# Kernel tuning notes

Hardware: AMD Instinct MI355X
Metric: run time of the kernel (lower is better)

Reference implementation:

```python
import jax, jax.numpy as jnp
import numpy as np

N = 512

def setup_inputs() -> dict:
    key = jax.random.key(0)
    ks = jax.random.split(key, 7)
    def rn(k, shape, fan_in):
        # kaiming-ish scale so activations stay sane
        return jax.random.normal(k, shape, dtype=jnp.float32) / np.sqrt(max(fan_in, 1))
    return {
        "x": jax.random.normal(ks[0], (N,), dtype=jnp.float32),
        "W1": rn(ks[1], (2, 1024), 2),
        "b1": rn(ks[2], (1024,), 1024),
        "W2": rn(ks[3], (1024, 128), 1024),
        "b2": rn(ks[4], (128,), 128),
        "W3": rn(ks[5], (128, 1), 128),
        "b3": rn(ks[6], (1,), 1),
    }


def reference(x, W1, b1, W2, b2, W3, b3):
    n = x.shape[0]
    # all (t_i, t_j) pairs: [N, N, 2]
    pairs = jnp.stack(
        [jnp.broadcast_to(x[:, None], (n, n)),
         jnp.broadcast_to(x[None, :], (n, n))], axis=-1)
    # batched 3-layer MLP over all pairs
    h = jax.nn.relu(jnp.einsum("ijc,ch->ijh", pairs, W1) + b1)   # [N,N,1024]
    h = jax.nn.relu(jnp.einsum("ijh,hk->ijk", h, W2) + b2)       # [N,N,128]
    out = (jnp.einsum("ijk,ko->ijo", h, W3) + b3)[..., 0]        # [N,N]
    # original fills only j >= i (diagonal overwritten from eye); lower stays 0
    K = jnp.triu(out)
    return K.T @ K
```

## Files before the change

### kernel.cpp

```cpp
#include <hip/hip_runtime.h>
#include <hip/hip_fp16.h>

typedef _Float16 f16;
typedef _Float16 f16x8 __attribute__((ext_vector_type(8)));
typedef float f32x4 __attribute__((ext_vector_type(4)));

__device__ __forceinline__ f16x8 relu8(f16x8 a) {
#if __has_builtin(__builtin_elementwise_max)
  return __builtin_elementwise_max(a, (f16x8)(f16)0);
#else
  f16x8 r;
#pragma unroll
  for (int i = 0; i < 8; i++) r[i] = a[i] > (f16)0 ? a[i] : (f16)0;
  return r;
#endif
}

__device__ __forceinline__ f16x8 bcast8(f16 s) {
  return (f16x8){s, s, s, s, s, s, s, s};
}

__global__ __launch_bounds__(512, 2) void k_fused(
    const float* __restrict__ x, const float* __restrict__ W1,
    const float* __restrict__ b1, const float* __restrict__ b2,
    const float* __restrict__ W3, const float* __restrict__ b3,
    const float* __restrict__ W2,
    float* __restrict__ Kp0, float* __restrict__ Kp1) {
  __shared__ f16 w2f[65536];
  __shared__ f16 w1af[1024], b1f[1024], w1bf[1024];
  __shared__ f16 hat[8192];
  __shared__ f16 xs[512];

  const int tid = threadIdx.x;
  const int lane = tid & 63, wv = tid >> 6;
  const int cL = lane & 15, q = lane >> 4;

  if (tid < 128) {
    const int c8 = tid << 3;
    const float4 a0 = *(const float4*)(W1 + c8);
    const float4 a1 = *(const float4*)(W1 + c8 + 4);
    const float4 g0 = *(const float4*)(b1 + c8);
    const float4 g1 = *(const float4*)(b1 + c8 + 4);
    f16x8 oa, og;
    oa[0] = (f16)a0.x; oa[1] = (f16)a0.y; oa[2] = (f16)a0.z; oa[3] = (f16)a0.w;
    oa[4] = (f16)a1.x; oa[5] = (f16)a1.y; oa[6] = (f16)a1.z; oa[7] = (f16)a1.w;
    og[0] = (f16)g0.x; og[1] = (f16)g0.y; og[2] = (f16)g0.z; og[3] = (f16)g0.w;
    og[4] = (f16)g1.x; og[5] = (f16)g1.y; og[6] = (f16)g1.z; og[7] = (f16)g1.w;
    *(f16x8*)(&w1af[c8]) = oa;
    *(f16x8*)(&b1f[c8]) = og;
  } else if (tid < 256) {
    const int c8 = (tid - 128) << 3;
    const float4 a0 = *(const float4*)(W1 + 1024 + c8);
    const float4 a1 = *(const float4*)(W1 + 1024 + c8 + 4);
    f16x8 ob;
    ob[0] = (f16)a0.x; ob[1] = (f16)a0.y; ob[2] = (f16)a0.z; ob[3] = (f16)a0.w;
    ob[4] = (f16)a1.x; ob[5] = (f16)a1.y; ob[6] = (f16)a1.z; ob[7] = (f16)a1.w;
    *(f16x8*)(&w1bf[c8]) = ob;
  } else if (tid < 320) {
    const int c8 = (tid - 256) << 3;
    const float4 x0 = *(const float4*)(x + c8);
    const float4 x1 = *(const float4*)(x + c8 + 4);
    f16x8 ox;
    ox[0] = (f16)x0.x; ox[1] = (f16)x0.y; ox[2] = (f16)x0.z; ox[3] = (f16)x0.w;
    ox[4] = (f16)x1.x; ox[5] = (f16)x1.y; ox[6] = (f16)x1.z; ox[7] = (f16)x1.w;
    *(f16x8*)(&xs[c8]) = ox;
  }

  int cur_nh = -1;

  for (int t = (int)blockIdx.x; t < 320; t += 256) {
    int nh, jt, s;
    if (t < 64 || t >= 256) {
      const int b = (t < 64) ? t : (t - 256);
      nh = b & 1;
      const int jd = b >> 1;
      const int jt1 = jd >> 4, l = jd & 15;
      if (t < 64) { jt = jt1;            s = jt * 16 + l; }
      else        { jt = (jt1 + 2) & 3;  s = jt * 16 + (15 - l); }
    } else {
      const int f = t - 64;
      nh = f & 1;
      const int jf = f >> 1;
      if (jf < 16)      { jt = 1; s = jf; }
      else if (jf < 48) { jt = 2; s = jf - 16; }
      else              { jt = 3; s = jf - 48; }
    }
    const int i0 = s << 3, j0 = jt << 7;
    float* __restrict__ Kp = nh ? Kp1 : Kp0;

    __syncthreads();
    if (nh != cur_nh) {
      #pragma unroll
      for (int p = 0; p < 16; p++) {
        const int sl = p * 512 + tid;
        const int frag = sl >> 6, l = sl & 63;
        const int cgL = frag >> 5, kb2 = frag & 31;
        const int q2 = l >> 4, cL2 = l & 15;
        const int n = nh * 64 + cgL * 16 + cL2;
        const float* src = W2 + (kb2 * 32 + q2 * 8) * 128 + n;
        f16x8 o;
        #pragma unroll
        for (int e = 0; e < 8; e++) o[e] = (f16)src[e * 128];
        *(f16x8*)(&w2f[frag * 512 + l * 8]) = o;
      }
      cur_nh = nh;
    }
    {
      const int il_s = tid >> 6, kb = (tid & 63) << 4;
      const f16x8 xv = bcast8(xs[i0 + il_s]);
      const f16x8 wa0 = *(const f16x8*)(&w1af[kb]);
      const f16x8 wa1 = *(const f16x8*)(&w1af[kb + 8]);
      const f16x8 bb0 = *(const f16x8*)(&b1f[kb]);
      const f16x8 bb1 = *(const f16x8*)(&b1f[kb + 8]);
      *(f16x8*)(&hat[il_s * 1024 + kb])     = xv * wa0 + bb0;
      *(f16x8*)(&hat[il_s * 1024 + kb + 8]) = xv * wa1 + bb1;
    }
    __syncthreads();

    const int i = i0 + wv;
    const int dij = i - j0;
    const int rgmin = (dij > 0) ? (dij >> 4) : 0;

    f16 xjs[8];
    #pragma unroll
    for (int rg = 0; rg < 8; rg++) xjs[rg] = xs[j0 + rg * 16 + cL];

    f32x4 acc[8][4];
    #pragma unroll
    for (int rg = 0; rg < 8; rg++)
      #pragma unroll
      for (int cg = 0; cg < 4; cg++) acc[rg][cg] = (f32x4){0.f, 0.f, 0.f, 0.f};

    const f16* hrow  = hat + wv * 1024 + q * 8;
    const f16* wrow  = w1bf + q * 8;
    const f16* bbase = w2f + lane * 8;

    for (int kk = 0; kk < 32; ++kk) {
      const f16x8 hv = *(const f16x8*)(hrow + kk * 32);
      const f16x8 wb = *(const f16x8*)(wrow + kk * 32);
      f16x8 bf[4];
      #pragma unroll
      for (int cg = 0; cg < 4; cg++)
        bf[cg] = *(const f16x8*)(bbase + (cg * 32 + kk) * 512);
      #pragma unroll
      for (int rg = 0; rg < 8; rg++) {
        if (rg >= rgmin) {
          const f16x8 af = relu8(bcast8(xjs[rg]) * wb + hv);
          #pragma unroll
          for (int cg = 0; cg < 4; cg++)
            acc[rg][cg] = __builtin_amdgcn_mfma_f32_16x16x32_f16(af, bf[cg], acc[rg][cg], 0, 0, 0);
        }
      }
    }

    float b2v[4], w3v[4];
    #pragma unroll
    for (int cg = 0; cg < 4; cg++) {
      b2v[cg] = b2[nh * 64 + cg * 16 + cL];
      w3v[cg] = W3[nh * 64 + cg * 16 + cL];
    }
    const float badd = (nh == 0) ? b3[0] : 0.f;
    #pragma unroll
    for (int rg = 0; rg < 8; rg++) {
      if (rg >= rgmin) {
        #pragma unroll
        for (int r = 0; r < 4; r++) {
          float ssum = 0.f;
          #pragma unroll
          for (int cg = 0; cg < 4; cg++)
            ssum = fmaf(fmaxf(acc[rg][cg][r] + b2v[cg], 0.f), w3v[cg], ssum);
          ssum += __shfl_xor(ssum, 1, 64);
          ssum += __shfl_xor(ssum, 2, 64);
          ssum += __shfl_xor(ssum, 4, 64);
          ssum += __shfl_xor(ssum, 8, 64);
          if (cL == 0) {
            const int j = j0 + rg * 16 + q * 4 + r;
            if (j >= i) Kp[i * 512 + j] = ssum + badd;
          }
        }
      }
    }
  }
}

__global__ __launch_bounds__(256) void k_atta2(const float* __restrict__ K0,
                                               const float* __restrict__ K1,
                                               float* __restrict__ C) {
  __shared__ __align__(16) float sp[2][32 * 36];
  __shared__ __align__(16) float sq[2][32 * 36];

  int a = 0, rem = (int)blockIdx.x;
  #pragma unroll
  for (int aa = 0; aa < 16; aa++) {
    const int c = 16 - aa;
    if (rem < c) { a = aa; break; }
    rem -= c;
  }
  const int b = a + rem;
  const int pb = a * 32, qb = b * 32;
  const int nchunk = a + 1;

  const int tid = threadIdx.x;
  const int ii = tid >> 3, p4 = (tid & 7) << 2;
  const int tx = tid & 15, ty = tid >> 4;

  float4 x0, x1, y0, y1;
  {
    const int gp = ii * 512 + pb + p4, gq = ii * 512 + qb + p4;
    x0 = *(const float4*)(K0 + gp);
    x1 = *(const float4*)(K1 + gp);
    y0 = *(const float4*)(K0 + gq);
    y1 = *(const float4*)(K1 + gq);
  }

  float c00 = 0.f, c01 = 0.f, c10 = 0.f, c11 = 0.f;

  for (int ic = 0; ic < nchunk; ic++) {
    float* __restrict__ spb = sp[ic & 1];
    float* __restrict__ sqb = sq[ic & 1];
    const int r = ic * 32 + ii;
    float4 vp, vq;
    vp.x = (r <= pb + p4 + 0) ? x0.x + x1.x : 0.f;
    vp.y = (r <= pb + p4 + 1) ? x0.y + x1.y : 0.f;
    vp.z = (r <= pb + p4 + 2) ? x0.z + x1.z : 0.f;
    vp.w = (r <= pb + p4 + 3) ? x0.w + x1.w : 0.f;
    vq.x = (r <= qb + p4 + 0) ? y0.x + y1.x : 0.f;
    vq.y = (r <= qb + p4 + 1) ? y0.y + y1.y : 0.f;
    vq.z = (r <= qb + p4 + 2) ? y0.z + y1.z : 0.f;
    vq.w = (r <= qb + p4 + 3) ? y0.w + y1.w : 0.f;
    *(float4*)&spb[ii * 36 + p4] = vp;
    *(float4*)&sqb[ii * 36 + p4] = vq;
    __syncthreads();

    if (ic + 1 < nchunk) {
      const int r2 = (ic + 1) * 32 + ii;
      const int gp = r2 * 512 + pb + p4, gq = r2 * 512 + qb + p4;
      x0 = *(const float4*)(K0 + gp);
      x1 = *(const float4*)(K1 + gp);
      y0 = *(const float4*)(K0 + gq);
      y1 = *(const float4*)(K1 + gq);
    }

    #pragma unroll 8
    for (int k = 0; k < 32; k++) {
      const float2 av = *(const float2*)&spb[k * 36 + ty * 2];
      const float2 bv = *(const float2*)&sqb[k * 36 + tx * 2];
      c00 = fmaf(av.x, bv.x, c00); c01 = fmaf(av.x, bv.y, c01);
      c10 = fmaf(av.y, bv.x, c10); c11 = fmaf(av.y, bv.y, c11);
    }
  }

  const int p0 = pb + ty * 2, q0 = qb + tx * 2;
  *(float2*)&C[p0 * 512 + q0]       = make_float2(c00, c01);
  *(float2*)&C[(p0 + 1) * 512 + q0] = make_float2(c10, c11);
  if (pb != qb) {
    *(float2*)&C[q0 * 512 + p0]       = make_float2(c00, c10);
    *(float2*)&C[(q0 + 1) * 512 + p0] = make_float2(c01, c11);
  }
}

extern "C" void kernel_launch(void* const* d_in, const int* in_sizes, int n_in,
                              void* d_out, int out_size, void* d_ws, size_t ws_size,
                              hipStream_t stream) {
  const float* x  = (const float*)d_in[0];
  const float* W1 = (const float*)d_in[1];
  const float* b1 = (const float*)d_in[2];
  const float* W2 = (const float*)d_in[3];
  const float* b2 = (const float*)d_in[4];
  const float* W3 = (const float*)d_in[5];
  const float* b3 = (const float*)d_in[6];
  float* out = (float*)d_out;
  char* ws = (char*)d_ws;

  float* Kp0 = (float*)ws;
  float* Kp1 = (float*)(ws + (1 << 20));

  k_fused<<<256, 512, 0, stream>>>(x, W1, b1, b2, W3, b3, W2, Kp0, Kp1);
  k_atta2<<<136, 256, 0, stream>>>(Kp0, Kp1, out);
}
```

Before: 119.2 us.

## Split MLP tile into two half passes with double-buffered LDS loads and MFMA priority

The 8x4 MFMA accumulator tile per wave is split into two sequential passes of 4x4, which halves accumulator register pressure and skips whole passes below the diagonal. Each pass software-pipelines its LDS loads (h, W1b, W2 fragments) one k-step ahead and raises wave priority around the MFMA groups. The cost is that W2 and h fragments are reloaded from LDS once per half, and the extra template specialisation adds code size.

Result: no change. 121.1 us (+1.6%).

```diff
diff --git a/kernel.cpp b/kernel.cpp
--- a/kernel.cpp
+++ b/kernel.cpp
@@ -2,6 +2,7 @@
 #include <hip/hip_fp16.h>
 
 typedef _Float16 f16;
+typedef _Float16 f16x4 __attribute__((ext_vector_type(4)));
 typedef _Float16 f16x8 __attribute__((ext_vector_type(8)));
 typedef float f32x4 __attribute__((ext_vector_type(4)));
 
@@ -18,6 +19,48 @@
 
 __device__ __forceinline__ f16x8 bcast8(f16 s) {
   return (f16x8){s, s, s, s, s, s, s, s};
+}
+
+struct Acc16 { f32x4 a[16]; };
+
+template <bool GUARD>
+__device__ __forceinline__ Acc16 mlp_pass(
+    const f16* __restrict__ hrow, const f16* __restrict__ wrow,
+    const f16* __restrict__ bbase, const f16x4 xj, const int rgeff) {
+  Acc16 A;
+#pragma unroll
+  for (int t = 0; t < 16; t++) A.a[t] = (f32x4){0.f, 0.f, 0.f, 0.f};
+
+  f16x8 hvb[2], wbb[2], bfb[2][4];
+  hvb[0] = *(const f16x8*)(hrow);
+  wbb[0] = *(const f16x8*)(wrow);
+#pragma unroll
+  for (int cg = 0; cg < 4; cg++)
+    bfb[0][cg] = *(const f16x8*)(bbase + (cg * 32) * 512);
+
+#pragma unroll 2
+  for (int kk = 0; kk < 32; ++kk) {
+    const int cur = kk & 1, nxt = cur ^ 1;
+    const int kn = (kk < 31) ? (kk + 1) : 31;
+    hvb[nxt] = *(const f16x8*)(hrow + kn * 32);
+    wbb[nxt] = *(const f16x8*)(wrow + kn * 32);
+#pragma unroll
+    for (int cg = 0; cg < 4; cg++)
+      bfb[nxt][cg] = *(const f16x8*)(bbase + (cg * 32 + kn) * 512);
+#pragma unroll
+    for (int rg = 0; rg < 4; rg++) {
+      if (!GUARD || rg >= rgeff) {
+        const f16x8 af = relu8(bcast8(xj[rg]) * wbb[cur] + hvb[cur]);
+        __builtin_amdgcn_s_setprio(1);
+#pragma unroll
+        for (int cg = 0; cg < 4; cg++)
+          A.a[rg * 4 + cg] = __builtin_amdgcn_mfma_f32_16x16x32_f16(
+              af, bfb[cur][cg], A.a[rg * 4 + cg], 0, 0, 0);
+        __builtin_amdgcn_s_setprio(0);
+      }
+    }
+  }
+  return A;
 }
 
 __global__ __launch_bounds__(512, 2) void k_fused(
@@ -121,37 +164,9 @@
     const int dij = i - j0;
     const int rgmin = (dij > 0) ? (dij >> 4) : 0;
 
-    f16 xjs[8];
-    #pragma unroll
-    for (int rg = 0; rg < 8; rg++) xjs[rg] = xs[j0 + rg * 16 + cL];
-
-    f32x4 acc[8][4];
-    #pragma unroll
-    for (int rg = 0; rg < 8; rg++)
-      #pragma unroll
-      for (int cg = 0; cg < 4; cg++) acc[rg][cg] = (f32x4){0.f, 0.f, 0.f, 0.f};
-
     const f16* hrow  = hat + wv * 1024 + q * 8;
     const f16* wrow  = w1bf + q * 8;
     const f16* bbase = w2f + lane * 8;
-
-    for (int kk = 0; kk < 32; ++kk) {
-      const f16x8 hv = *(const f16x8*)(hrow + kk * 32);
-      const f16x8 wb = *(const f16x8*)(wrow + kk * 32);
-      f16x8 bf[4];
-      #pragma unroll
-      for (int cg = 0; cg < 4; cg++)
-        bf[cg] = *(const f16x8*)(bbase + (cg * 32 + kk) * 512);
-      #pragma unroll
-      for (int rg = 0; rg < 8; rg++) {
-        if (rg >= rgmin) {
-          const f16x8 af = relu8(bcast8(xjs[rg]) * wb + hv);
-          #pragma unroll
-          for (int cg = 0; cg < 4; cg++)
-            acc[rg][cg] = __builtin_amdgcn_mfma_f32_16x16x32_f16(af, bf[cg], acc[rg][cg], 0, 0, 0);
-        }
-      }
-    }
 
     float b2v[4], w3v[4];
     #pragma unroll
@@ -160,22 +175,36 @@
       w3v[cg] = W3[nh * 64 + cg * 16 + cL];
     }
     const float badd = (nh == 0) ? b3[0] : 0.f;
-    #pragma unroll
-    for (int rg = 0; rg < 8; rg++) {
-      if (rg >= rgmin) {
-        #pragma unroll
-        for (int r = 0; r < 4; r++) {
-          float ssum = 0.f;
+
+    for (int half = 0; half < 2; ++half) {
+      const int rb = half << 2;
+      if (rgmin >= rb + 4) continue;
+
+      f16x4 xj;
+      #pragma unroll
+      for (int rg = 0; rg < 4; rg++) xj[rg] = xs[j0 + (rb + rg) * 16 + cL];
+
+      Acc16 A = (rgmin <= rb)
+                    ? mlp_pass<false>(hrow, wrow, bbase, xj, 0)
+                    : mlp_pass<true>(hrow, wrow, bbase, xj, rgmin - rb);
+
+      #pragma unroll
+      for (int rg = 0; rg < 4; rg++) {
+        if (rb + rg >= rgmin) {
           #pragma unroll
-          for (int cg = 0; cg < 4; cg++)
-            ssum = fmaf(fmaxf(acc[rg][cg][r] + b2v[cg], 0.f), w3v[cg], ssum);
-          ssum += __shfl_xor(ssum, 1, 64);
-          ssum += __shfl_xor(ssum, 2, 64);
-          ssum += __shfl_xor(ssum, 4, 64);
-          ssum += __shfl_xor(ssum, 8, 64);
-          if (cL == 0) {
-            const int j = j0 + rg * 16 + q * 4 + r;
-            if (j >= i) Kp[i * 512 + j] = ssum + badd;
+          for (int r = 0; r < 4; r++) {
+            float ssum = 0.f;
+            #pragma unroll
+            for (int cg = 0; cg < 4; cg++)
+              ssum = fmaf(fmaxf(A.a[rg * 4 + cg][r] + b2v[cg], 0.f), w3v[cg], ssum);
+            ssum += __shfl_xor(ssum, 1, 64);
+            ssum += __shfl_xor(ssum, 2, 64);
+            ssum += __shfl_xor(ssum, 4, 64);
+            ssum += __shfl_xor(ssum, 8, 64);
+            if (cL == 0) {
+              const int j = j0 + (rb + rg) * 16 + q * 4 + r;
+              if (j >= i) Kp[i * 512 + j] = ssum + badd;
+            }
           }
         }
       }
```

## Split N-columns of fused MLP across two waves per row with LDS reduction

Applied to the files above, without the earlier changes.

Doubles the block size to 1024 threads so each row i is handled by two waves, each computing half of the 64 output columns (2 MFMA column groups instead of 4). Partial layer-3 dot products are written to shared memory (reusing the hat buffer) and summed by one wave before the store. This halves accumulator registers per wave and doubles wave-level parallelism to hide MFMA and LDS latency. The cost is an extra barrier and an LDS reduction per tile, and the relu'd A fragment is now recomputed by both waves.

Measured after the change: 134.4 us. 1.13x slower.

```diff
diff --git a/kernel.cpp b/kernel.cpp
--- a/kernel.cpp
+++ b/kernel.cpp
@@ -20,7 +20,7 @@
   return (f16x8){s, s, s, s, s, s, s, s};
 }
 
-__global__ __launch_bounds__(512, 2) void k_fused(
+__global__ __launch_bounds__(1024, 4) void k_fused(
     const float* __restrict__ x, const float* __restrict__ W1,
     const float* __restrict__ b1, const float* __restrict__ b2,
     const float* __restrict__ W3, const float* __restrict__ b3,
@@ -32,7 +32,10 @@
   __shared__ f16 xs[512];
 
   const int tid = threadIdx.x;
-  const int lane = tid & 63, wv = tid >> 6;
+  const int lane = tid & 63;
+  const int wv16 = tid >> 6;
+  const int il = wv16 >> 1;
+  const int cgh = wv16 & 1;
   const int cL = lane & 15, q = lane >> 4;
 
   if (tid < 128) {
@@ -91,8 +94,8 @@
     __syncthreads();
     if (nh != cur_nh) {
       #pragma unroll
-      for (int p = 0; p < 16; p++) {
-        const int sl = p * 512 + tid;
+      for (int p = 0; p < 8; p++) {
+        const int sl = p * 1024 + tid;
         const int frag = sl >> 6, l = sl & 63;
         const int cgL = frag >> 5, kb2 = frag & 31;
         const int q2 = l >> 4, cL2 = l & 15;
@@ -106,18 +109,15 @@
       cur_nh = nh;
     }
     {
-      const int il_s = tid >> 6, kb = (tid & 63) << 4;
+      const int il_s = tid >> 7, kb = (tid & 127) << 3;
       const f16x8 xv = bcast8(xs[i0 + il_s]);
-      const f16x8 wa0 = *(const f16x8*)(&w1af[kb]);
-      const f16x8 wa1 = *(const f16x8*)(&w1af[kb + 8]);
-      const f16x8 bb0 = *(const f16x8*)(&b1f[kb]);
-      const f16x8 bb1 = *(const f16x8*)(&b1f[kb + 8]);
-      *(f16x8*)(&hat[il_s * 1024 + kb])     = xv * wa0 + bb0;
-      *(f16x8*)(&hat[il_s * 1024 + kb + 8]) = xv * wa1 + bb1;
-    }
-    __syncthreads();
-
-    const int i = i0 + wv;
+      const f16x8 wa = *(const f16x8*)(&w1af[kb]);
+      const f16x8 bb = *(const f16x8*)(&b1f[kb]);
+      *(f16x8*)(&hat[il_s * 1024 + kb]) = xv * wa + bb;
+    }
+    __syncthreads();
+
+    const int i = i0 + il;
     const int dij = i - j0;
     const int rgmin = (dij > 0) ? (dij >> 4) : 0;
 
@@ -125,59 +125,69 @@
     #pragma unroll
     for (int rg = 0; rg < 8; rg++) xjs[rg] = xs[j0 + rg * 16 + cL];
 
-    f32x4 acc[8][4];
-    #pragma unroll
-    for (int rg = 0; rg < 8; rg++)
-      #pragma unroll
-      for (int cg = 0; cg < 4; cg++) acc[rg][cg] = (f32x4){0.f, 0.f, 0.f, 0.f};
-
-    const f16* hrow  = hat + wv * 1024 + q * 8;
+    f32x4 acc[8][2];
+    #pragma unroll
+    for (int rg = 0; rg < 8; rg++) {
+      acc[rg][0] = (f32x4){0.f, 0.f, 0.f, 0.f};
+      acc[rg][1] = (f32x4){0.f, 0.f, 0.f, 0.f};
+    }
+
+    const f16* hrow  = hat + il * 1024 + q * 8;
     const f16* wrow  = w1bf + q * 8;
-    const f16* bbase = w2f + lane * 8;
+    const f16* bbase = w2f + cgh * 32768 + lane * 8;
 
     for (int kk = 0; kk < 32; ++kk) {
       const f16x8 hv = *(const f16x8*)(hrow + kk * 32);
       const f16x8 wb = *(const f16x8*)(wrow + kk * 32);
-      f16x8 bf[4];
-      #pragma unroll
-      for (int cg = 0; cg < 4; cg++)
-        bf[cg] = *(const f16x8*)(bbase + (cg * 32 + kk) * 512);
+      const f16x8 bf0 = *(const f16x8*)(bbase + kk * 512);
+      const f16x8 bf1 = *(const f16x8*)(bbase + 16384 + kk * 512);
       #pragma unroll
       for (int rg = 0; rg < 8; rg++) {
         if (rg >= rgmin) {
           const f16x8 af = relu8(bcast8(xjs[rg]) * wb + hv);
-          #pragma unroll
-          for (int cg = 0; cg < 4; cg++)
-            acc[rg][cg] = __builtin_amdgcn_mfma_f32_16x16x32_f16(af, bf[cg], acc[rg][cg], 0, 0, 0);
+          acc[rg][0] = __builtin_amdgcn_mfma_f32_16x16x32_f16(af, bf0, acc[rg][0], 0, 0, 0);
+          acc[rg][1] = __builtin_amdgcn_mfma_f32_16x16x32_f16(af, bf1, acc[rg][1], 0, 0, 0);
         }
       }
     }
 
-    float b2v[4], w3v[4];
-    #pragma unroll
-    for (int cg = 0; cg < 4; cg++) {
-      b2v[cg] = b2[nh * 64 + cg * 16 + cL];
-      w3v[cg] = W3[nh * 64 + cg * 16 + cL];
-    }
-    const float badd = (nh == 0) ? b3[0] : 0.f;
+    float b2v[2], w3v[2];
+    #pragma unroll
+    for (int c = 0; c < 2; c++) {
+      const int n = nh * 64 + (cgh * 2 + c) * 16 + cL;
+      b2v[c] = b2[n];
+      w3v[c] = W3[n];
+    }
+
+    __syncthreads();
+    float* part = (float*)hat;
+
     #pragma unroll
     for (int rg = 0; rg < 8; rg++) {
       if (rg >= rgmin) {
         #pragma unroll
         for (int r = 0; r < 4; r++) {
-          float ssum = 0.f;
-          #pragma unroll
-          for (int cg = 0; cg < 4; cg++)
-            ssum = fmaf(fmaxf(acc[rg][cg][r] + b2v[cg], 0.f), w3v[cg], ssum);
+          float ssum = fmaf(fmaxf(acc[rg][0][r] + b2v[0], 0.f), w3v[0],
+                       fmaxf(acc[rg][1][r] + b2v[1], 0.f) * w3v[1]);
           ssum += __shfl_xor(ssum, 1, 64);
           ssum += __shfl_xor(ssum, 2, 64);
           ssum += __shfl_xor(ssum, 4, 64);
           ssum += __shfl_xor(ssum, 8, 64);
-          if (cL == 0) {
-            const int j = j0 + rg * 16 + q * 4 + r;
-            if (j >= i) Kp[i * 512 + j] = ssum + badd;
-          }
+          if (cL == 0)
+            part[(cgh * 8 + il) * 128 + rg * 16 + q * 4 + r] = ssum;
         }
+      }
+    }
+    __syncthreads();
+
+    if (cgh == 0) {
+      const float badd = (nh == 0) ? b3[0] : 0.f;
+      #pragma unroll
+      for (int jj0 = 0; jj0 < 128; jj0 += 64) {
+        const int jj = jj0 + lane;
+        const int j = j0 + jj;
+        if (j >= i)
+          Kp[i * 512 + j] = part[il * 128 + jj] + part[(8 + il) * 128 + jj] + badd;
       }
     }
   }
@@ -275,6 +285,6 @@
   float* Kp0 = (float*)ws;
   float* Kp1 = (float*)(ws + (1 << 20));
 
-  k_fused<<<256, 512, 0, stream>>>(x, W1, b1, b2, W3, b3, W2, Kp0, Kp1);
+  k_fused<<<256, 1024, 0, stream>>>(x, W1, b1, b2, W3, b3, W2, Kp0, Kp1);
   k_atta2<<<136, 256, 0, stream>>>(Kp0, Kp1, out);
 }
```

## Replace per-pair MLP with piecewise-linear sweep over sorted x breakpoints

Applied to the files above, without the earlier changes.

For a fixed i, the first-layer activation of each hidden unit is piecewise linear in x_j and has a single ReLU breakpoint. The new code sorts x once in a prep kernel, then builds per-row event lists of hidden units bucketed by breakpoint. A sweep across the sorted x_j keeps running prefix sums A and B of the W2 columns, so the second layer costs O(1024·128) per row instead of one MFMA GEMM per pair. This removes the dense fp16 MFMA work and the two-half partial K buffers. In exchange it adds a bitonic sort, atomics-based bucketing, a serial sweep whose work differs between waves, scattered stores back to unsorted column positions, and fp32 accumulation order that differs from the reference.

New measurement: 295.3 us. 2.48x slower.

```diff
diff --git a/kernel.cpp b/kernel.cpp
--- a/kernel.cpp
+++ b/kernel.cpp
@@ -2,195 +2,251 @@
 #include <hip/hip_fp16.h>
 
 typedef _Float16 f16;
+typedef _Float16 f16x2 __attribute__((ext_vector_type(2)));
 typedef _Float16 f16x8 __attribute__((ext_vector_type(8)));
-typedef float f32x4 __attribute__((ext_vector_type(4)));
-
-__device__ __forceinline__ f16x8 relu8(f16x8 a) {
-#if __has_builtin(__builtin_elementwise_max)
-  return __builtin_elementwise_max(a, (f16x8)(f16)0);
-#else
-  f16x8 r;
-#pragma unroll
-  for (int i = 0; i < 8; i++) r[i] = a[i] > (f16)0 ? a[i] : (f16)0;
-  return r;
-#endif
+
+#define WS_XS 0
+#define WS_JO 2048
+#define WS_W2H 4096
+#define WS_K (1 << 19)
+
+__global__ __launch_bounds__(512) void k_prep(const float* __restrict__ x,
+                                              const float* __restrict__ W2,
+                                              char* __restrict__ ws) {
+  __shared__ float xv[512];
+  __shared__ int xj[512];
+  const int tid = threadIdx.x;
+  xv[tid] = x[tid];
+  xj[tid] = tid;
+  __syncthreads();
+  for (int k2 = 2; k2 <= 512; k2 <<= 1) {
+    for (int j2 = k2 >> 1; j2 >= 1; j2 >>= 1) {
+      const int partner = tid ^ j2;
+      if (partner > tid) {
+        const bool asc = ((tid & k2) == 0);
+        const float a = xv[tid], b = xv[partner];
+        const bool sw = asc ? (a > b) : (a < b);
+        if (sw) {
+          xv[tid] = b; xv[partner] = a;
+          const int ja = xj[tid]; xj[tid] = xj[partner]; xj[partner] = ja;
+        }
+      }
+      __syncthreads();
+    }
+  }
+  ((float*)(ws + WS_XS))[tid] = xv[tid];
+  ((int*)(ws + WS_JO))[tid] = xj[tid];
+
+  f16* __restrict__ w2h = (f16*)(ws + WS_W2H);
+  for (int base = tid * 8; base < 1024 * 128; base += 512 * 8) {
+    const float4 a = *(const float4*)(W2 + base);
+    const float4 b = *(const float4*)(W2 + base + 4);
+    f16x8 o;
+    o[0] = (f16)a.x; o[1] = (f16)a.y; o[2] = (f16)a.z; o[3] = (f16)a.w;
+    o[4] = (f16)b.x; o[5] = (f16)b.y; o[6] = (f16)b.z; o[7] = (f16)b.w;
+    *(f16x8*)(w2h + base) = o;
+  }
 }
 
-__device__ __forceinline__ f16x8 bcast8(f16 s) {
-  return (f16x8){s, s, s, s, s, s, s, s};
-}
-
-__global__ __launch_bounds__(512, 2) void k_fused(
+__global__ __launch_bounds__(256, 2) void k_sweep(
     const float* __restrict__ x, const float* __restrict__ W1,
     const float* __restrict__ b1, const float* __restrict__ b2,
     const float* __restrict__ W3, const float* __restrict__ b3,
-    const float* __restrict__ W2,
-    float* __restrict__ Kp0, float* __restrict__ Kp1) {
-  __shared__ f16 w2f[65536];
-  __shared__ f16 w1af[1024], b1f[1024], w1bf[1024];
-  __shared__ f16 hat[8192];
-  __shared__ f16 xs[512];
+    const char* __restrict__ ws, float* __restrict__ Kf) {
+  __shared__ float xsp[512];
+  __shared__ int jof[512];
+  __shared__ float evc[2048], evt[2048];
+  __shared__ unsigned short evk[2048];
+  __shared__ int startS[513];
+  __shared__ int histS[513];
+  __shared__ float chkA[4][128], chkB[4][128];
+  __shared__ float outls[512];
 
   const int tid = threadIdx.x;
   const int lane = tid & 63, wv = tid >> 6;
-  const int cL = lane & 15, q = lane >> 4;
-
-  if (tid < 128) {
-    const int c8 = tid << 3;
-    const float4 a0 = *(const float4*)(W1 + c8);
-    const float4 a1 = *(const float4*)(W1 + c8 + 4);
-    const float4 g0 = *(const float4*)(b1 + c8);
-    const float4 g1 = *(const float4*)(b1 + c8 + 4);
-    f16x8 oa, og;
-    oa[0] = (f16)a0.x; oa[1] = (f16)a0.y; oa[2] = (f16)a0.z; oa[3] = (f16)a0.w;
-    oa[4] = (f16)a1.x; oa[5] = (f16)a1.y; oa[6] = (f16)a1.z; oa[7] = (f16)a1.w;
-    og[0] = (f16)g0.x; og[1] = (f16)g0.y; og[2] = (f16)g0.z; og[3] = (f16)g0.w;
-    og[4] = (f16)g1.x; og[5] = (f16)g1.y; og[6] = (f16)g1.z; og[7] = (f16)g1.w;
-    *(f16x8*)(&w1af[c8]) = oa;
-    *(f16x8*)(&b1f[c8]) = og;
-  } else if (tid < 256) {
-    const int c8 = (tid - 128) << 3;
-    const float4 a0 = *(const float4*)(W1 + 1024 + c8);
-    const float4 a1 = *(const float4*)(W1 + 1024 + c8 + 4);
-    f16x8 ob;
-    ob[0] = (f16)a0.x; ob[1] = (f16)a0.y; ob[2] = (f16)a0.z; ob[3] = (f16)a0.w;
-    ob[4] = (f16)a1.x; ob[5] = (f16)a1.y; ob[6] = (f16)a1.z; ob[7] = (f16)a1.w;
-    *(f16x8*)(&w1bf[c8]) = ob;
-  } else if (tid < 320) {
-    const int c8 = (tid - 256) << 3;
-    const float4 x0 = *(const float4*)(x + c8);
-    const float4 x1 = *(const float4*)(x + c8 + 4);
-    f16x8 ox;
-    ox[0] = (f16)x0.x; ox[1] = (f16)x0.y; ox[2] = (f16)x0.z; ox[3] = (f16)x0.w;
-    ox[4] = (f16)x1.x; ox[5] = (f16)x1.y; ox[6] = (f16)x1.z; ox[7] = (f16)x1.w;
-    *(f16x8*)(&xs[c8]) = ox;
-  }
-
-  int cur_nh = -1;
-
-  for (int t = (int)blockIdx.x; t < 320; t += 256) {
-    int nh, jt, s;
-    if (t < 64 || t >= 256) {
-      const int b = (t < 64) ? t : (t - 256);
-      nh = b & 1;
-      const int jd = b >> 1;
-      const int jt1 = jd >> 4, l = jd & 15;
-      if (t < 64) { jt = jt1;            s = jt * 16 + l; }
-      else        { jt = (jt1 + 2) & 3;  s = jt * 16 + (15 - l); }
-    } else {
-      const int f = t - 64;
-      nh = f & 1;
-      const int jf = f >> 1;
-      if (jf < 16)      { jt = 1; s = jf; }
-      else if (jf < 48) { jt = 2; s = jf - 16; }
-      else              { jt = 3; s = jf - 48; }
-    }
-    const int i0 = s << 3, j0 = jt << 7;
-    float* __restrict__ Kp = nh ? Kp1 : Kp0;
-
-    __syncthreads();
-    if (nh != cur_nh) {
-      #pragma unroll
-      for (int p = 0; p < 16; p++) {
-        const int sl = p * 512 + tid;
-        const int frag = sl >> 6, l = sl & 63;
-        const int cgL = frag >> 5, kb2 = frag & 31;
-        const int q2 = l >> 4, cL2 = l & 15;
-        const int n = nh * 64 + cgL * 16 + cL2;
-        const float* src = W2 + (kb2 * 32 + q2 * 8) * 128 + n;
-        f16x8 o;
-        #pragma unroll
-        for (int e = 0; e < 8; e++) o[e] = (f16)src[e * 128];
-        *(f16x8*)(&w2f[frag * 512 + l * 8]) = o;
-      }
-      cur_nh = nh;
-    }
-    {
-      const int il_s = tid >> 6, kb = (tid & 63) << 4;
-      const f16x8 xv = bcast8(xs[i0 + il_s]);
-      const f16x8 wa0 = *(const f16x8*)(&w1af[kb]);
-      const f16x8 wa1 = *(const f16x8*)(&w1af[kb + 8]);
-      const f16x8 bb0 = *(const f16x8*)(&b1f[kb]);
-      const f16x8 bb1 = *(const f16x8*)(&b1f[kb + 8]);
-      *(f16x8*)(&hat[il_s * 1024 + kb])     = xv * wa0 + bb0;
-      *(f16x8*)(&hat[il_s * 1024 + kb + 8]) = xv * wa1 + bb1;
-    }
-    __syncthreads();
-
-    const int i = i0 + wv;
-    const int dij = i - j0;
-    const int rgmin = (dij > 0) ? (dij >> 4) : 0;
-
-    f16 xjs[8];
-    #pragma unroll
-    for (int rg = 0; rg < 8; rg++) xjs[rg] = xs[j0 + rg * 16 + cL];
-
-    f32x4 acc[8][4];
-    #pragma unroll
-    for (int rg = 0; rg < 8; rg++)
-      #pragma unroll
-      for (int cg = 0; cg < 4; cg++) acc[rg][cg] = (f32x4){0.f, 0.f, 0.f, 0.f};
-
-    const f16* hrow  = hat + wv * 1024 + q * 8;
-    const f16* wrow  = w1bf + q * 8;
-    const f16* bbase = w2f + lane * 8;
-
-    for (int kk = 0; kk < 32; ++kk) {
-      const f16x8 hv = *(const f16x8*)(hrow + kk * 32);
-      const f16x8 wb = *(const f16x8*)(wrow + kk * 32);
-      f16x8 bf[4];
-      #pragma unroll
-      for (int cg = 0; cg < 4; cg++)
-        bf[cg] = *(const f16x8*)(bbase + (cg * 32 + kk) * 512);
-      #pragma unroll
-      for (int rg = 0; rg < 8; rg++) {
-        if (rg >= rgmin) {
-          const f16x8 af = relu8(bcast8(xjs[rg]) * wb + hv);
-          #pragma unroll
-          for (int cg = 0; cg < 4; cg++)
-            acc[rg][cg] = __builtin_amdgcn_mfma_f32_16x16x32_f16(af, bf[cg], acc[rg][cg], 0, 0, 0);
+  const int i = (int)blockIdx.x;
+  const float xi = x[i];
+  const f16* __restrict__ w2h = (const f16*)(ws + WS_W2H);
+
+  {
+    const float* xsg = (const float*)(ws + WS_XS);
+    const int* jog = (const int*)(ws + WS_JO);
+    xsp[tid] = xsg[tid];       xsp[tid + 256] = xsg[tid + 256];
+    jof[tid] = jog[tid];       jof[tid + 256] = jog[tid + 256];
+    histS[tid] = 0;            histS[tid + 256] = 0;
+    if (tid == 0) histS[512] = 0;
+  }
+  __syncthreads();
+
+  float kc[4], kt[4];
+  int kpos[4];
+#pragma unroll
+  for (int r = 0; r < 4; r++) {
+    const int k = tid + 256 * r;
+    const float a = W1[k], c = W1[1024 + k], b = b1[k];
+    const float t = fmaf(a, xi, b);
+    kc[r] = c; kt[r] = t;
+    int pos = 0;
+    if (c != 0.f) {
+      const float bp = -t / c;
+#pragma unroll
+      for (int s = 256; s > 0; s >>= 1)
+        if (pos + s <= 512 && xsp[pos + s - 1] < bp) pos += s;
+    }
+    kpos[r] = pos;
+    if (c > 0.f) {
+      atomicAdd(&histS[pos], 1);
+    } else if (c < 0.f) {
+      atomicAdd(&histS[0], 1);
+      atomicAdd(&histS[pos], 1);
+    } else if (t > 0.f) {
+      atomicAdd(&histS[0], 1);
+    }
+  }
+  __syncthreads();
+
+  if (wv == 0) {
+    int hloc[8], s8 = 0;
+#pragma unroll
+    for (int u = 0; u < 8; u++) { hloc[u] = histS[lane * 8 + u]; s8 += hloc[u]; }
+    int incl = s8;
+#pragma unroll
+    for (int d = 1; d < 64; d <<= 1) {
+      const int o = __shfl_up(incl, d, 64);
+      if (lane >= d) incl += o;
+    }
+    int run = incl - s8;
+#pragma unroll
+    for (int u = 0; u < 8; u++) { startS[lane * 8 + u] = run; run += hloc[u]; }
+    if (lane == 63) startS[512] = incl;
+  }
+  __syncthreads();
+  histS[tid] = startS[tid];
+  histS[tid + 256] = startS[tid + 256];
+  if (tid == 0) histS[512] = startS[512];
+  __syncthreads();
+
+#pragma unroll
+  for (int r = 0; r < 4; r++) {
+    const int k = tid + 256 * r;
+    const float c = kc[r], t = kt[r];
+    if (c > 0.f) {
+      const int sl = atomicAdd(&histS[kpos[r]], 1);
+      evc[sl] = c; evt[sl] = t; evk[sl] = (unsigned short)k;
+    } else if (c < 0.f) {
+      int sl = atomicAdd(&histS[0], 1);
+      evc[sl] = c; evt[sl] = t; evk[sl] = (unsigned short)k;
+      sl = atomicAdd(&histS[kpos[r]], 1);
+      evc[sl] = -c; evt[sl] = -t; evk[sl] = (unsigned short)k;
+    } else if (t > 0.f) {
+      const int sl = atomicAdd(&histS[0], 1);
+      evc[sl] = 0.f; evt[sl] = t; evk[sl] = (unsigned short)k;
+    }
+  }
+  __syncthreads();
+
+  const int n0 = 2 * lane;
+  const float b2n0 = b2[n0], b2n1 = b2[n0 + 1];
+  const float w3n0 = W3[n0], w3n1 = W3[n0 + 1];
+
+  const int csBeg = startS[wv * 128];
+  const int csEnd = startS[(wv + 1) * 128];
+
+  {
+    float dA0 = 0.f, dB0 = 0.f, dA1 = 0.f, dB1 = 0.f;
+    for (int e = csBeg; e < csEnd; e += 8) {
+      float pc[8], pt[8], pw0[8], pw1[8];
+#pragma unroll
+      for (int u = 0; u < 8; u++) {
+        const int idx = min(e + u, 2047);
+        pc[u] = evc[idx]; pt[u] = evt[idx];
+        const int k = evk[idx] & 1023;
+        const f16x2 wp = *(const f16x2*)(w2h + k * 128 + n0);
+        pw0[u] = (float)wp[0]; pw1[u] = (float)wp[1];
+      }
+#pragma unroll
+      for (int u = 0; u < 8; u++) {
+        if (e + u < csEnd) {
+          dA0 = fmaf(pc[u], pw0[u], dA0); dB0 = fmaf(pt[u], pw0[u], dB0);
+          dA1 = fmaf(pc[u], pw1[u], dA1); dB1 = fmaf(pt[u], pw1[u], dB1);
         }
       }
     }
-
-    float b2v[4], w3v[4];
-    #pragma unroll
-    for (int cg = 0; cg < 4; cg++) {
-      b2v[cg] = b2[nh * 64 + cg * 16 + cL];
-      w3v[cg] = W3[nh * 64 + cg * 16 + cL];
-    }
-    const float badd = (nh == 0) ? b3[0] : 0.f;
-    #pragma unroll
-    for (int rg = 0; rg < 8; rg++) {
-      if (rg >= rgmin) {
-        #pragma unroll
-        for (int r = 0; r < 4; r++) {
-          float ssum = 0.f;
-          #pragma unroll
-          for (int cg = 0; cg < 4; cg++)
-            ssum = fmaf(fmaxf(acc[rg][cg][r] + b2v[cg], 0.f), w3v[cg], ssum);
-          ssum += __shfl_xor(ssum, 1, 64);
-          ssum += __shfl_xor(ssum, 2, 64);
-          ssum += __shfl_xor(ssum, 4, 64);
-          ssum += __shfl_xor(ssum, 8, 64);
-          if (cL == 0) {
-            const int j = j0 + rg * 16 + q * 4 + r;
-            if (j >= i) Kp[i * 512 + j] = ssum + badd;
+    chkA[wv][n0] = dA0; chkA[wv][n0 + 1] = dA1;
+    chkB[wv][n0] = dB0; chkB[wv][n0 + 1] = dB1;
+  }
+  __syncthreads();
+
+  float A0 = 0.f, B0 = 0.f, A1 = 0.f, B1 = 0.f;
+  for (int u = 0; u < wv; u++) {
+    A0 += chkA[u][n0]; A1 += chkA[u][n0 + 1];
+    B0 += chkB[u][n0]; B1 += chkB[u][n0 + 1];
+  }
+
+  {
+    int p = wv * 128;
+    const int p1 = p + 128;
+    int e = csBeg;
+    const int eEnd = csEnd;
+    int nextB = startS[p + 1];
+
+    auto EMIT = [&](int pp) {
+      const float xp = xsp[pp];
+      float v = fmaxf(fmaf(A0, xp, B0) + b2n0, 0.f) * w3n0 +
+                fmaxf(fmaf(A1, xp, B1) + b2n1, 0.f) * w3n1;
+#pragma unroll
+      for (int d = 1; d < 64; d <<= 1) v += __shfl_xor(v, d, 64);
+      if (lane == 0) outls[pp] = v;
+    };
+
+    while (p < p1) {
+      while (p < p1 && nextB <= e) {
+        EMIT(p); p++;
+        if (p < p1) nextB = startS[p + 1];
+      }
+      if (p >= p1) break;
+      float pc[8], pt[8], pw0[8], pw1[8];
+#pragma unroll
+      for (int u = 0; u < 8; u++) {
+        const int idx = min(e + u, 2047);
+        pc[u] = evc[idx]; pt[u] = evt[idx];
+        const int k = evk[idx] & 1023;
+        const f16x2 wp = *(const f16x2*)(w2h + k * 128 + n0);
+        pw0[u] = (float)wp[0]; pw1[u] = (float)wp[1];
+      }
+#pragma unroll
+      for (int u = 0; u < 8; u++) {
+        if (e + u >= nextB) {
+          while (p < p1 && nextB <= e + u) {
+            EMIT(p); p++;
+            if (p < p1) nextB = startS[p + 1];
           }
         }
-      }
-    }
+        if (e + u < eEnd) {
+          A0 = fmaf(pc[u], pw0[u], A0); B0 = fmaf(pt[u], pw0[u], B0);
+          A1 = fmaf(pc[u], pw1[u], A1); B1 = fmaf(pt[u], pw1[u], B1);
+        }
+      }
+      e += 8;
+    }
+  }
+  __syncthreads();
+
+  const float b3v = b3[0];
+#pragma unroll
+  for (int r = 0; r < 2; r++) {
+    const int pp = tid + 256 * r;
+    Kf[i * 512 + jof[pp]] = outls[pp] + b3v;
   }
 }
 
-__global__ __launch_bounds__(256) void k_atta2(const float* __restrict__ K0,
-                                               const float* __restrict__ K1,
-                                               float* __restrict__ C) {
+__global__ __launch_bounds__(256) void k_ktk(const float* __restrict__ K0,
+                                             float* __restrict__ C) {
   __shared__ __align__(16) float sp[2][32 * 36];
   __shared__ __align__(16) float sq[2][32 * 36];
 
   int a = 0, rem = (int)blockIdx.x;
-  #pragma unroll
+#pragma unroll
   for (int aa = 0; aa < 16; aa++) {
     const int c = 16 - aa;
     if (rem < c) { a = aa; break; }
@@ -204,13 +260,11 @@
   const int ii = tid >> 3, p4 = (tid & 7) << 2;
   const int tx = tid & 15, ty = tid >> 4;
 
-  float4 x0, x1, y0, y1;
+  float4 x0, y0;
   {
     const int gp = ii * 512 + pb + p4, gq = ii * 512 + qb + p4;
     x0 = *(const float4*)(K0 + gp);
-    x1 = *(const float4*)(K1 + gp);
     y0 = *(const float4*)(K0 + gq);
-    y1 = *(const float4*)(K1 + gq);
   }
 
   float c00 = 0.f, c01 = 0.f, c10 = 0.f, c11 = 0.f;
@@ -220,14 +274,14 @@
     float* __restrict__ sqb = sq[ic & 1];
     const int r = ic * 32 + ii;
     float4 vp, vq;
-    vp.x = (r <= pb + p4 + 0) ? x0.x + x1.x : 0.f;
-    vp.y = (r <= pb + p4 + 1) ? x0.y + x1.y : 0.f;
-    vp.z = (r <= pb + p4 + 2) ? x0.z + x1.z : 0.f;
-    vp.w = (r <= pb + p4 + 3) ? x0.w + x1.w : 0.f;
-    vq.x = (r <= qb + p4 + 0) ? y0.x + y1.x : 0.f;
-    vq.y = (r <= qb + p4 + 1) ? y0.y + y1.y : 0.f;
-    vq.z = (r <= qb + p4 + 2) ? y0.z + y1.z : 0.f;
-    vq.w = (r <= qb + p4 + 3) ? y0.w + y1.w : 0.f;
+    vp.x = (r <= pb + p4 + 0) ? x0.x : 0.f;
+    vp.y = (r <= pb + p4 + 1) ? x0.y : 0.f;
+    vp.z = (r <= pb + p4 + 2) ? x0.z : 0.f;
+    vp.w = (r <= pb + p4 + 3) ? x0.w : 0.f;
+    vq.x = (r <= qb + p4 + 0) ? y0.x : 0.f;
+    vq.y = (r <= qb + p4 + 1) ? y0.y : 0.f;
+    vq.z = (r <= qb + p4 + 2) ? y0.z : 0.f;
+    vq.w = (r <= qb + p4 + 3) ? y0.w : 0.f;
     *(float4*)&spb[ii * 36 + p4] = vp;
     *(float4*)&sqb[ii * 36 + p4] = vq;
     __syncthreads();
@@ -236,12 +290,10 @@
       const int r2 = (ic + 1) * 32 + ii;
       const int gp = r2 * 512 + pb + p4, gq = r2 * 512 + qb + p4;
       x0 = *(const float4*)(K0 + gp);
-      x1 = *(const float4*)(K1 + gp);
       y0 = *(const float4*)(K0 + gq);
-      y1 = *(const float4*)(K1 + gq);
-    }
-
-    #pragma unroll 8
+    }
+
+#pragma unroll 8
     for (int k = 0; k < 32; k++) {
       const float2 av = *(const float2*)&spb[k * 36 + ty * 2];
       const float2 bv = *(const float2*)&sqb[k * 36 + tx * 2];
@@ -271,10 +323,9 @@
   const float* b3 = (const float*)d_in[6];
   float* out = (float*)d_out;
   char* ws = (char*)d_ws;
-
-  float* Kp0 = (float*)ws;
-  float* Kp1 = (float*)(ws + (1 << 20));
-
-  k_fused<<<256, 512, 0, stream>>>(x, W1, b1, b2, W3, b3, W2, Kp0, Kp1);
-  k_atta2<<<136, 256, 0, stream>>>(Kp0, Kp1, out);
+  float* Kf = (float*)(ws + WS_K);
+
+  k_prep<<<1, 512, 0, stream>>>(x, W2, ws);
+  k_sweep<<<512, 256, 0, stream>>>(x, W1, b1, b2, W3, b3, ws, Kf);
+  k_ktk<<<136, 256, 0, stream>>>(Kf, out);
 }
```
